# Optimization experiments

Hardware: AMD Instinct MI355X
Metric: run time of the kernel (lower is better)

## Reference

```python
import jax, jax.numpy as jnp
import numpy as np

B, G, GS = 1024, 2000, 25   # batch, num gene groups, group size
H1, H2, C = 1024, 512, 10
EPS = 1e-5


def _xavier(key, shape, fan_in, fan_out):
    lim = np.sqrt(6.0 / (fan_in + fan_out))
    return jax.random.uniform(key, shape, jnp.float32, -lim, lim)


def setup_inputs() -> dict:
    key = jax.random.key(0)
    ks = jax.random.split(key, 8)
    x = jax.random.normal(ks[0], (B, G * GS), jnp.float32)
    # per-group Linear(GS, 1) weights stacked -> block-diagonal grouped GEMM
    gene_w = _xavier(ks[1], (G, GS), GS, 1)
    gene_b = jnp.zeros((G,), jnp.float32)
    W1 = _xavier(ks[2], (G, H1), G, H1)
    b1 = jnp.zeros((H1,), jnp.float32)
    W2 = _xavier(ks[3], (H1, H2), H1, H2)
    b2 = jnp.zeros((H2,), jnp.float32)
    Wout = _xavier(ks[4], (H2, C), H2, C)
    bout = jnp.zeros((C,), jnp.float32)
    Wres = _xavier(ks[5], (G, C), G, C)
    bres = jnp.zeros((C,), jnp.float32)
    gamma1 = jnp.ones((H1,), jnp.float32); beta1 = jnp.zeros((H1,), jnp.float32)
    gamma2 = jnp.ones((H2,), jnp.float32); beta2 = jnp.zeros((H2,), jnp.float32)
    return dict(x=x, gene_w=gene_w, gene_b=gene_b, W1=W1, b1=b1,
                gamma1=gamma1, beta1=beta1, W2=W2, b2=b2,
                gamma2=gamma2, beta2=beta2, Wout=Wout, bout=bout,
                Wres=Wres, bres=bres)


def _batch_norm(h, gamma, beta):
    # training-mode BatchNorm1d: biased batch statistics over axis 0
    mu = jnp.mean(h, axis=0)
    var = jnp.mean(jnp.square(h - mu), axis=0)
    return gamma * (h - mu) * jax.lax.rsqrt(var + EPS) + beta


def reference(x, gene_w, gene_b, W1, b1, gamma1, beta1, W2, b2,
              gamma2, beta2, Wout, bout, Wres, bres):
    # fused replacement for the per-group Linear(GS,1)+ReLU loop + cat
    xg = x.reshape(B, G, GS)
    g = jax.nn.relu(jnp.einsum('bgk,gk->bg', xg, gene_w) + gene_b)  # [B, G]
    h1 = jax.nn.relu(_batch_norm(g @ W1 + b1, gamma1, beta1))       # [B, H1]
    h2 = jax.nn.relu(_batch_norm(h1 @ W2 + b2, gamma2, beta2))      # [B, H2]
    x_main = h2 @ Wout + bout                                       # [B, C]
    x_res = g @ Wres + bres                                         # [B, C]
    return jax.nn.softmax(x_main + x_res, axis=1)
```

## Files before the change

kernel.cpp:

```cpp
#include <hip/hip_runtime.h>
#include <math.h>

#define NB   1024
#define NG   2000
#define NGS  25
#define KP   2048
#define NH1  1024
#define NH2  512
#define NC   10
#define EPSV 1e-5f
#define GPB  200


typedef __attribute__((ext_vector_type(8)))  __bf16 bf16x8;
typedef __attribute__((ext_vector_type(4)))  float  f32x4;
typedef __attribute__((ext_vector_type(16))) float  f32x16;
typedef __attribute__((ext_vector_type(8)))  unsigned short u16x8;
typedef __attribute__((ext_vector_type(4)))  unsigned short u16x4;

__device__ __forceinline__ unsigned short f2bf(float f) {
  union { float f; unsigned u; } v; v.f = f;
  return (unsigned short)((v.u + 0x7fffu + ((v.u >> 16) & 1u)) >> 16);
}
__device__ __forceinline__ float bf2f(unsigned short b) {
  union { unsigned u; float f; } v; v.u = ((unsigned)b) << 16;
  return v.f;
}

__global__ __launch_bounds__(256) void prep_kernel(
    const float* __restrict__ x, const float* __restrict__ gw,
    const float* __restrict__ gb, unsigned short* __restrict__ g_bf,
    const float* __restrict__ W1, unsigned short* __restrict__ W1bT,
    const float* __restrict__ W2, unsigned short* __restrict__ W2bT,
    float* __restrict__ stats) {
  __shared__ char smem[GPB * NGS * 4];
  int t = threadIdx.x;

  if (blockIdx.y < 10) {
    float* xs = (float*)smem;
    int b = blockIdx.x;
    int blk = blockIdx.y;
    const float4* src = (const float4*)(x + (size_t)b * (NG * NGS) + blk * (GPB * NGS));
    float4* dst = (float4*)xs;
    for (int i = t; i < (GPB * NGS) / 4; i += 256) dst[i] = src[i];
    __syncthreads();
    if (t < GPB) {
      int gi = blk * GPB + t;
      const float* wp = gw + gi * NGS;
      const float* xp = xs + t * NGS;
      float acc = 0.f;
#pragma unroll
      for (int k = 0; k < NGS; ++k) acc = fmaf(xp[k], wp[k], acc);
      acc += gb[gi];
      g_bf[(size_t)b * KP + gi] = f2bf(fmaxf(acc, 0.f));
    } else if (blk == 9 && t < GPB + (KP - NG)) {
      g_bf[(size_t)b * KP + NG + (t - GPB)] = 0;
    }
    return;
  }

  int bx = blockIdx.x;
  if (bx == 640) {
    for (int i = t; i < 3072; i += 256) stats[i] = 0.f;
    return;
  }
  const float* src; unsigned short* dst; int K, N, Kpad, k0, n0;
  if (bx < 512)      { src = W1; dst = W1bT; K = NG;  N = NH1; Kpad = KP;
                       k0 = (bx & 31) * 64; n0 = (bx >> 5) * 64; }
  else if (bx < 640) { int xi = bx - 512;
                       src = W2; dst = W2bT; K = NH1; N = NH2; Kpad = NH1;
                       k0 = (xi & 15) * 64; n0 = (xi >> 4) * 64; }
  else return;

  unsigned short (*ts)[72] = (unsigned short (*)[72])smem;
  int c4 = (t & 15) * 4;
  int r  = t >> 4;
  for (int rr = r; rr < 64; rr += 16) {
    int k = k0 + rr;
    float4 v = make_float4(0.f, 0.f, 0.f, 0.f);
    if (k < K) v = *(const float4*)&src[(size_t)k * N + n0 + c4];
    ts[rr][c4 + 0] = f2bf(v.x); ts[rr][c4 + 1] = f2bf(v.y);
    ts[rr][c4 + 2] = f2bf(v.z); ts[rr][c4 + 3] = f2bf(v.w);
  }
  __syncthreads();
  int rr8 = (t & 7) * 8;
  int cc  = t >> 3;
  for (int c = cc; c < 64; c += 32) {
    u16x8 val;
#pragma unroll
    for (int i = 0; i < 8; ++i) val[i] = ts[rr8 + i][c];
    *(u16x8*)&dst[(size_t)(n0 + c) * Kpad + k0 + rr8] = val;
  }
}

__global__ __launch_bounds__(256) void gemm1_kernel(
    const unsigned short* __restrict__ A,
    const unsigned short* __restrict__ Bt,
    float* __restrict__ C, float* __restrict__ sum, float* __restrict__ sq,
    int M, int N, int Kp) {
  __shared__ unsigned short As[32][68];
  __shared__ unsigned short Bs[64][68];
  __shared__ float ebuf[2 * 64 * 17];
  int t = threadIdx.x;
  int m0 = blockIdx.y * 32, n0 = blockIdx.x * 64;
  int wave = t >> 6, lane = t & 63;
  int h = wave & 1;
  int p = wave >> 1;
  int l31 = lane & 31, l5 = lane >> 5;
  int srow = t >> 3, skc = (t & 7) * 8;

  f32x16 acc;
#pragma unroll
  for (int q = 0; q < 16; ++q) acc[q] = 0.f;

  const unsigned short* Ap = A + (size_t)(m0 + srow) * Kp + skc;
  const unsigned short* Bp = Bt + (size_t)(n0 + srow) * Kp + skc;
  size_t rstep = 32 * (size_t)Kp;

  u16x8 pa0 = *(const u16x8*)(Ap);
  u16x8 pb0 = *(const u16x8*)(Bp);
  u16x8 pb1 = *(const u16x8*)(Bp + rstep);

  for (int k0 = 0; k0 < Kp; k0 += 64) {
    *(u16x8*)&As[srow][skc]      = pa0;
    *(u16x8*)&Bs[srow][skc]      = pb0;
    *(u16x8*)&Bs[srow + 32][skc] = pb1;
    __syncthreads();
    if (k0 + 64 < Kp) {
      pa0 = *(const u16x8*)(Ap + k0 + 64);
      pb0 = *(const u16x8*)(Bp + k0 + 64);
      pb1 = *(const u16x8*)(Bp + k0 + 64 + rstep);
    }
    int kb = p * 32 + l5 * 8;
    {
      bf16x8 av = *(const bf16x8*)&As[l31][kb];
      bf16x8 bv = *(const bf16x8*)&Bs[h * 32 + l31][kb];
      acc = __builtin_amdgcn_mfma_f32_32x32x16_bf16(av, bv, acc, 0, 0, 0);
    }
    {
      bf16x8 av = *(const bf16x8*)&As[l31][kb + 16];
      bf16x8 bv = *(const bf16x8*)&Bs[h * 32 + l31][kb + 16];
      acc = __builtin_amdgcn_mfma_f32_32x32x16_bf16(av, bv, acc, 0, 0, 0);
    }
    __syncthreads();
  }

  float* eb = ebuf + (size_t)(h * 64 + lane) * 17;
  if (p == 1) {
#pragma unroll
    for (int r = 0; r < 16; ++r) eb[r] = acc[r];
  }
  __syncthreads();
  if (p == 0) {
    float s = 0.f, ss = 0.f;
#pragma unroll
    for (int r = 0; r < 16; ++r) {
      float v = acc[r] + eb[r];
      int row = m0 + (r & 3) + 8 * (r >> 2) + 4 * l5;
      C[(size_t)row * N + n0 + h * 32 + l31] = v;
      s += v;
      ss = fmaf(v, v, ss);
    }
    s  += __shfl_down(s, 32, 64);
    ss += __shfl_down(ss, 32, 64);
    if (lane < 32) {
      atomicAdd(&sum[n0 + h * 32 + lane], s);
      atomicAdd(&sq[n0 + h * 32 + lane], ss);
    }
  }
}

__global__ __launch_bounds__(256) void gemm2_kernel(
    const float* __restrict__ A,
    const unsigned short* __restrict__ Bt,
    float* __restrict__ C, const float* __restrict__ sum1,
    const float* __restrict__ sq1, const float* __restrict__ gam1,
    const float* __restrict__ bet1, float* __restrict__ sum2,
    float* __restrict__ sq2, int M, int N, int Kp) {
  __shared__ unsigned short As[32][72];
  __shared__ unsigned short Bs[32][72];
  int t = threadIdx.x;
  int m0 = blockIdx.y * 32, n0 = blockIdx.x * 32;
  int wave = t >> 6, lane = t & 63;
  int wm = (wave >> 1) * 16, wn = (wave & 1) * 16;
  int fm = lane & 15, fk = (lane >> 4) * 8;
  int srow = t >> 3, skc = (t & 7) * 8;

  f32x4 acc = (f32x4){0.f, 0.f, 0.f, 0.f};

  const float* Ap = A + (size_t)(m0 + srow) * Kp + skc;
  const unsigned short* Bp = Bt + (size_t)(n0 + srow) * Kp + skc;

  f32x4 pa0 = *(const f32x4*)(Ap);
  f32x4 pa1 = *(const f32x4*)(Ap + 4);
  u16x8 pb0 = *(const u16x8*)(Bp);

  for (int k0 = 0; k0 < Kp; k0 += 64) {
    float sc[8], sh[8];
#pragma unroll
    for (int i = 0; i < 8; ++i) {
      int k = k0 + skc + i;
      float mu  = sum1[k] * (1.f / NB);
      float var = sq1[k] * (1.f / NB) - mu * mu;
      float rs  = rsqrtf(var + EPSV);
      sc[i] = gam1[k] * rs;
      sh[i] = fmaf(-mu, sc[i], bet1[k]);
    }
    u16x8 a0;
#pragma unroll
    for (int i = 0; i < 4; ++i) {
      a0[i]     = f2bf(fmaxf(fmaf(pa0[i], sc[i],     sh[i]),     0.f));
      a0[i + 4] = f2bf(fmaxf(fmaf(pa1[i], sc[i + 4], sh[i + 4]), 0.f));
    }
    *(u16x8*)&As[srow][skc] = a0;
    *(u16x8*)&Bs[srow][skc] = pb0;
    __syncthreads();
    if (k0 + 64 < Kp) {
      pa0 = *(const f32x4*)(Ap + k0 + 64);
      pa1 = *(const f32x4*)(Ap + k0 + 64 + 4);
      pb0 = *(const u16x8*)(Bp + k0 + 64);
    }
#pragma unroll
    for (int s = 0; s < 2; ++s) {
      bf16x8 af = *(const bf16x8*)&As[wm + fm][s * 32 + fk];
      bf16x8 bf = *(const bf16x8*)&Bs[wn + fm][s * 32 + fk];
      acc = __builtin_amdgcn_mfma_f32_16x16x32_bf16(af, bf, acc, 0, 0, 0);
    }
    __syncthreads();
  }

  int crow = (lane >> 4) * 4, ccol = lane & 15;
  float s = 0.f, ss = 0.f;
#pragma unroll
  for (int r = 0; r < 4; ++r) {
    float v = acc[r];
    int m = m0 + wm + crow + r;
    int n = n0 + wn + ccol;
    C[(size_t)m * N + n] = v;
    s += v;
    ss = fmaf(v, v, ss);
  }
  s  += __shfl_down(s, 32, 64);  s  += __shfl_down(s, 16, 64);
  ss += __shfl_down(ss, 32, 64); ss += __shfl_down(ss, 16, 64);
  if (lane < 16) {
    atomicAdd(&sum2[n0 + wn + lane], s);
    atomicAdd(&sq2[n0 + wn + lane], ss);
  }
}

__global__ __launch_bounds__(256) void final_kernel(
    const float* __restrict__ t2, const float* __restrict__ sum2,
    const float* __restrict__ sq2, const float* __restrict__ gam2,
    const float* __restrict__ bet2, const unsigned short* __restrict__ g_bf,
    const float* __restrict__ Wout, const float* __restrict__ bout,
    const float* __restrict__ Wres, const float* __restrict__ bres,
    float* __restrict__ out) {
  int b = blockIdx.x;
  int t = threadIdx.x;
  float acc[NC] = {};

  if (t < NH2 / 4) {
    float4 tv = *(const float4*)&t2[(size_t)b * NH2 + t * 4];
    float raw[4] = {tv.x, tv.y, tv.z, tv.w};
    float hr[4];
#pragma unroll
    for (int i = 0; i < 4; ++i) {
      int c = t * 4 + i;
      float mu  = sum2[c] * (1.f / NB);
      float var = sq2[c] * (1.f / NB) - mu * mu;
      float rs  = rsqrtf(var + EPSV);
      float scv = gam2[c] * rs;
      hr[i] = fmaxf(fmaf(raw[i], scv, fmaf(-mu, scv, bet2[c])), 0.f);
    }
    const float4* wp = (const float4*)&Wout[t * 4 * NC];
    float w[40];
#pragma unroll
    for (int q = 0; q < 10; ++q) {
      float4 wv = wp[q];
      w[q * 4] = wv.x; w[q * 4 + 1] = wv.y; w[q * 4 + 2] = wv.z; w[q * 4 + 3] = wv.w;
    }
#pragma unroll
    for (int r = 0; r < 4; ++r)
#pragma unroll
      for (int c = 0; c < NC; ++c) acc[c] = fmaf(hr[r], w[r * NC + c], acc[c]);
  }

  for (int u = t; u < NG / 4; u += 256) {
    u16x4 gv = *(const u16x4*)&g_bf[(size_t)b * KP + u * 4];
    float gr[4] = {bf2f(gv[0]), bf2f(gv[1]), bf2f(gv[2]), bf2f(gv[3])};
    const float4* wp = (const float4*)&Wres[u * 4 * NC];
    float w[40];
#pragma unroll
    for (int q = 0; q < 10; ++q) {
      float4 wv = wp[q];
      w[q * 4] = wv.x; w[q * 4 + 1] = wv.y; w[q * 4 + 2] = wv.z; w[q * 4 + 3] = wv.w;
    }
#pragma unroll
    for (int r = 0; r < 4; ++r)
#pragma unroll
      for (int c = 0; c < NC; ++c) acc[c] = fmaf(gr[r], w[r * NC + c], acc[c]);
  }

  __shared__ float red[4][NC];
  __shared__ float logits[NC];
  int lane = t & 63, wave = t >> 6;
#pragma unroll
  for (int c = 0; c < NC; ++c) {
    float v = acc[c];
    for (int off = 32; off > 0; off >>= 1) v += __shfl_down(v, off, 64);
    if (lane == 0) red[wave][c] = v;
  }
  __syncthreads();
  if (t < NC)
    logits[t] = red[0][t] + red[1][t] + red[2][t] + red[3][t] + bout[t] + bres[t];
  __syncthreads();
  if (t == 0) {
    float mx = logits[0];
#pragma unroll
    for (int c = 1; c < NC; ++c) mx = fmaxf(mx, logits[c]);
    float e[NC], s = 0.f;
#pragma unroll
    for (int c = 0; c < NC; ++c) { e[c] = expf(logits[c] - mx); s += e[c]; }
    float inv = 1.f / s;
#pragma unroll
    for (int c = 0; c < NC; ++c) out[(size_t)b * NC + c] = e[c] * inv;
  }
}

extern "C" void kernel_launch(void* const* d_in, const int* in_sizes, int n_in,
                              void* d_out, int out_size, void* d_ws, size_t ws_size,
                              hipStream_t stream) {
  const float* x      = (const float*)d_in[0];
  const float* gw     = (const float*)d_in[1];
  const float* gb     = (const float*)d_in[2];
  const float* W1     = (const float*)d_in[3];
  const float* gamma1 = (const float*)d_in[5];
  const float* beta1  = (const float*)d_in[6];
  const float* W2     = (const float*)d_in[7];
  const float* gamma2 = (const float*)d_in[9];
  const float* beta2  = (const float*)d_in[10];
  const float* Wout   = (const float*)d_in[11];
  const float* bout   = (const float*)d_in[12];
  const float* Wres   = (const float*)d_in[13];
  const float* bres   = (const float*)d_in[14];
  float* out = (float*)d_out;

  char* p = (char*)d_ws;
  unsigned short* g_bf = (unsigned short*)p; p += (size_t)NB * KP * 2;
  unsigned short* W1bT = (unsigned short*)p; p += (size_t)NH1 * KP * 2;
  unsigned short* W2bT = (unsigned short*)p; p += (size_t)NH2 * NH1 * 2;
  float* t1 = (float*)p; p += (size_t)NB * NH1 * 4;
  float* t2 = (float*)p; p += (size_t)NB * NH2 * 4;
  float* stats = (float*)p;
  float* sum1 = stats, *sq1 = stats + 1024, *sum2 = stats + 2048, *sq2 = stats + 2560;

  prep_kernel<<<dim3(NB, 11), 256, 0, stream>>>(x, gw, gb, g_bf,
                                                W1, W1bT, W2, W2bT, stats);

  gemm1_kernel<<<dim3(NH1 / 64, NB / 32), 256, 0, stream>>>(
      g_bf, W1bT, t1, sum1, sq1, NB, NH1, KP);

  gemm2_kernel<<<dim3(NH2 / 32, NB / 32), 256, 0, stream>>>(
      t1, W2bT, t2, sum1, sq1, gamma1, beta1, sum2, sq2, NB, NH2, NH1);

  final_kernel<<<NB, 256, 0, stream>>>(t2, sum2, sq2, gamma2, beta2, g_bf,
                                       Wout, bout, Wres, bres, out);
}
```

Baseline: 364.8 us.

## Fuse residual projection into prep kernel and cache BN params in shared memory

The residual g@Wres product is now computed in the prep kernel while g is still in registers, in fp32. Each block writes partial logits per batch row, and the final kernel sums them instead of re-reading g_bf and all of Wres. gemm2 computes BN1 scale and shift once per block into shared memory rather than recomputing rsqrt in every k-iteration, and the final kernel stages Wout in LDS. This adds extra syncs and a Wres tile load in each prep block, plus a small partials buffer.

```diff
diff --git a/kernel.cpp b/kernel.cpp
--- a/kernel.cpp
+++ b/kernel.cpp
@@ -32,8 +32,10 @@
     const float* __restrict__ gb, unsigned short* __restrict__ g_bf,
     const float* __restrict__ W1, unsigned short* __restrict__ W1bT,
     const float* __restrict__ W2, unsigned short* __restrict__ W2bT,
+    const float* __restrict__ Wres, float* __restrict__ rp,
     float* __restrict__ stats) {
-  __shared__ char smem[GPB * NGS * 4];
+  __shared__ __attribute__((aligned(16))) char smem[GPB * NGS * 4];
+  __shared__ float rred[4][NC];
   int t = threadIdx.x;
 
   if (blockIdx.y < 10) {
@@ -44,6 +46,7 @@
     float4* dst = (float4*)xs;
     for (int i = t; i < (GPB * NGS) / 4; i += 256) dst[i] = src[i];
     __syncthreads();
+    float g = 0.f;
     if (t < GPB) {
       int gi = blk * GPB + t;
       const float* wp = gw + gi * NGS;
@@ -51,11 +54,31 @@
       float acc = 0.f;
 #pragma unroll
       for (int k = 0; k < NGS; ++k) acc = fmaf(xp[k], wp[k], acc);
-      acc += gb[gi];
-      g_bf[(size_t)b * KP + gi] = f2bf(fmaxf(acc, 0.f));
+      g = fmaxf(acc + gb[gi], 0.f);
+      g_bf[(size_t)b * KP + gi] = f2bf(g);
     } else if (blk == 9 && t < GPB + (KP - NG)) {
       g_bf[(size_t)b * KP + NG + (t - GPB)] = 0;
     }
+    __syncthreads();
+    float* ws = xs;
+    const float4* wsrc = (const float4*)(Wres + (size_t)blk * (GPB * NC));
+    float4* wdst = (float4*)ws;
+    for (int i = t; i < (GPB * NC) / 4; i += 256) wdst[i] = wsrc[i];
+    __syncthreads();
+    float r[NC];
+#pragma unroll
+    for (int c = 0; c < NC; ++c) r[c] = (t < GPB) ? g * ws[t * NC + c] : 0.f;
+    int lane = t & 63, wave = t >> 6;
+#pragma unroll
+    for (int c = 0; c < NC; ++c) {
+      float v = r[c];
+      for (int off = 32; off > 0; off >>= 1) v += __shfl_down(v, off, 64);
+      if (lane == 0) rred[wave][c] = v;
+    }
+    __syncthreads();
+    if (t < NC)
+      rp[(size_t)b * (10 * NC) + blk * NC + t] =
+          rred[0][t] + rred[1][t] + rred[2][t] + rred[3][t];
     return;
   }
 
@@ -179,6 +202,7 @@
     float* __restrict__ sq2, int M, int N, int Kp) {
   __shared__ unsigned short As[32][72];
   __shared__ unsigned short Bs[32][72];
+  __shared__ float sc1s[NH1], sh1s[NH1];
   int t = threadIdx.x;
   int m0 = blockIdx.y * 32, n0 = blockIdx.x * 32;
   int wave = t >> 6, lane = t & 63;
@@ -186,6 +210,14 @@
   int fm = lane & 15, fk = (lane >> 4) * 8;
   int srow = t >> 3, skc = (t & 7) * 8;
 
+  for (int k = t; k < Kp; k += 256) {
+    float mu  = sum1[k] * (1.f / NB);
+    float var = sq1[k] * (1.f / NB) - mu * mu;
+    float scv = gam1[k] * rsqrtf(var + EPSV);
+    sc1s[k] = scv;
+    sh1s[k] = fmaf(-mu, scv, bet1[k]);
+  }
+
   f32x4 acc = (f32x4){0.f, 0.f, 0.f, 0.f};
 
   const float* Ap = A + (size_t)(m0 + srow) * Kp + skc;
@@ -194,23 +226,18 @@
   f32x4 pa0 = *(const f32x4*)(Ap);
   f32x4 pa1 = *(const f32x4*)(Ap + 4);
   u16x8 pb0 = *(const u16x8*)(Bp);
+  __syncthreads();
 
   for (int k0 = 0; k0 < Kp; k0 += 64) {
-    float sc[8], sh[8];
-#pragma unroll
-    for (int i = 0; i < 8; ++i) {
-      int k = k0 + skc + i;
-      float mu  = sum1[k] * (1.f / NB);
-      float var = sq1[k] * (1.f / NB) - mu * mu;
-      float rs  = rsqrtf(var + EPSV);
-      sc[i] = gam1[k] * rs;
-      sh[i] = fmaf(-mu, sc[i], bet1[k]);
-    }
+    f32x4 scl = *(const f32x4*)&sc1s[k0 + skc];
+    f32x4 sch = *(const f32x4*)&sc1s[k0 + skc + 4];
+    f32x4 shl = *(const f32x4*)&sh1s[k0 + skc];
+    f32x4 shh = *(const f32x4*)&sh1s[k0 + skc + 4];
     u16x8 a0;
 #pragma unroll
     for (int i = 0; i < 4; ++i) {
-      a0[i]     = f2bf(fmaxf(fmaf(pa0[i], sc[i],     sh[i]),     0.f));
-      a0[i + 4] = f2bf(fmaxf(fmaf(pa1[i], sc[i + 4], sh[i + 4]), 0.f));
+      a0[i]     = f2bf(fmaxf(fmaf(pa0[i], scl[i], shl[i]), 0.f));
+      a0[i + 4] = f2bf(fmaxf(fmaf(pa1[i], sch[i], shh[i]), 0.f));
     }
     *(u16x8*)&As[srow][skc] = a0;
     *(u16x8*)&Bs[srow][skc] = pb0;
@@ -251,58 +278,36 @@
 __global__ __launch_bounds__(256) void final_kernel(
     const float* __restrict__ t2, const float* __restrict__ sum2,
     const float* __restrict__ sq2, const float* __restrict__ gam2,
-    const float* __restrict__ bet2, const unsigned short* __restrict__ g_bf,
+    const float* __restrict__ bet2, const float* __restrict__ rp,
     const float* __restrict__ Wout, const float* __restrict__ bout,
-    const float* __restrict__ Wres, const float* __restrict__ bres,
-    float* __restrict__ out) {
+    const float* __restrict__ bres, float* __restrict__ out) {
+  __shared__ __attribute__((aligned(16))) float wl[NH2 * NC];
+  __shared__ float red[4][NC];
+  __shared__ float logits[NC];
   int b = blockIdx.x;
   int t = threadIdx.x;
+
+  const float4* wsrc = (const float4*)Wout;
+  float4* wdst = (float4*)wl;
+#pragma unroll
+  for (int i = 0; i < (NH2 * NC / 4) / 256; ++i)
+    wdst[t + i * 256] = wsrc[t + i * 256];
+  __syncthreads();
+
   float acc[NC] = {};
-
-  if (t < NH2 / 4) {
-    float4 tv = *(const float4*)&t2[(size_t)b * NH2 + t * 4];
-    float raw[4] = {tv.x, tv.y, tv.z, tv.w};
-    float hr[4];
-#pragma unroll
-    for (int i = 0; i < 4; ++i) {
-      int c = t * 4 + i;
-      float mu  = sum2[c] * (1.f / NB);
-      float var = sq2[c] * (1.f / NB) - mu * mu;
-      float rs  = rsqrtf(var + EPSV);
-      float scv = gam2[c] * rs;
-      hr[i] = fmaxf(fmaf(raw[i], scv, fmaf(-mu, scv, bet2[c])), 0.f);
-    }
-    const float4* wp = (const float4*)&Wout[t * 4 * NC];
-    float w[40];
-#pragma unroll
-    for (int q = 0; q < 10; ++q) {
-      float4 wv = wp[q];
-      w[q * 4] = wv.x; w[q * 4 + 1] = wv.y; w[q * 4 + 2] = wv.z; w[q * 4 + 3] = wv.w;
-    }
-#pragma unroll
-    for (int r = 0; r < 4; ++r)
-#pragma unroll
-      for (int c = 0; c < NC; ++c) acc[c] = fmaf(hr[r], w[r * NC + c], acc[c]);
-  }
-
-  for (int u = t; u < NG / 4; u += 256) {
-    u16x4 gv = *(const u16x4*)&g_bf[(size_t)b * KP + u * 4];
-    float gr[4] = {bf2f(gv[0]), bf2f(gv[1]), bf2f(gv[2]), bf2f(gv[3])};
-    const float4* wp = (const float4*)&Wres[u * 4 * NC];
-    float w[40];
-#pragma unroll
-    for (int q = 0; q < 10; ++q) {
-      float4 wv = wp[q];
-      w[q * 4] = wv.x; w[q * 4 + 1] = wv.y; w[q * 4 + 2] = wv.z; w[q * 4 + 3] = wv.w;
-    }
-#pragma unroll
-    for (int r = 0; r < 4; ++r)
-#pragma unroll
-      for (int c = 0; c < NC; ++c) acc[c] = fmaf(gr[r], w[r * NC + c], acc[c]);
-  }
-
-  __shared__ float red[4][NC];
-  __shared__ float logits[NC];
+#pragma unroll
+  for (int half = 0; half < 2; ++half) {
+    int h = t + half * 256;
+    float raw = t2[(size_t)b * NH2 + h];
+    float mu  = sum2[h] * (1.f / NB);
+    float var = sq2[h] * (1.f / NB) - mu * mu;
+    float scv = gam2[h] * rsqrtf(var + EPSV);
+    float hr  = fmaxf(fmaf(raw, scv, fmaf(-mu, scv, bet2[h])), 0.f);
+    const float* wrow = &wl[h * NC];
+#pragma unroll
+    for (int c = 0; c < NC; ++c) acc[c] = fmaf(hr, wrow[c], acc[c]);
+  }
+
   int lane = t & 63, wave = t >> 6;
 #pragma unroll
   for (int c = 0; c < NC; ++c) {
@@ -311,8 +316,13 @@
     if (lane == 0) red[wave][c] = v;
   }
   __syncthreads();
-  if (t < NC)
-    logits[t] = red[0][t] + red[1][t] + red[2][t] + red[3][t] + bout[t] + bres[t];
+  if (t < NC) {
+    float v = red[0][t] + red[1][t] + red[2][t] + red[3][t] + bout[t] + bres[t];
+    const float* rpb = rp + (size_t)b * (10 * NC);
+#pragma unroll
+    for (int kb = 0; kb < 10; ++kb) v += rpb[kb * NC + t];
+    logits[t] = v;
+  }
   __syncthreads();
   if (t == 0) {
     float mx = logits[0];
@@ -351,11 +361,13 @@
   unsigned short* W2bT = (unsigned short*)p; p += (size_t)NH2 * NH1 * 2;
   float* t1 = (float*)p; p += (size_t)NB * NH1 * 4;
   float* t2 = (float*)p; p += (size_t)NB * NH2 * 4;
-  float* stats = (float*)p;
+  float* stats = (float*)p; p += 3072 * 4;
+  float* rp = (float*)p; p += (size_t)NB * 10 * NC * 4;
   float* sum1 = stats, *sq1 = stats + 1024, *sum2 = stats + 2048, *sq2 = stats + 2560;
 
   prep_kernel<<<dim3(NB, 11), 256, 0, stream>>>(x, gw, gb, g_bf,
-                                                W1, W1bT, W2, W2bT, stats);
+                                                W1, W1bT, W2, W2bT,
+                                                Wres, rp, stats);
 
   gemm1_kernel<<<dim3(NH1 / 64, NB / 32), 256, 0, stream>>>(
       g_bf, W1bT, t1, sum1, sq1, NB, NH1, KP);
@@ -363,6 +375,6 @@
   gemm2_kernel<<<dim3(NH2 / 32, NB / 32), 256, 0, stream>>>(
       t1, W2bT, t2, sum1, sq1, gamma1, beta1, sum2, sq2, NB, NH2, NH1);
 
-  final_kernel<<<NB, 256, 0, stream>>>(t2, sum2, sq2, gamma2, beta2, g_bf,
-                                       Wout, bout, Wres, bres, out);
-}
+  final_kernel<<<NB, 256, 0, stream>>>(t2, sum2, sq2, gamma2, beta2, rp,
+                                       Wout, bout, bres, out);
+}
```

New measurement: 362.3 us. Within noise of the previous version (-0.7%).
